# Kernel optimization log

Hardware: AMD Instinct MI355X
Metric: run time of the kernel (lower is better)

Reference implementation:

```python
import jax, jax.numpy as jnp
import numpy as np

B, T, D, H = 4, 1024, 1024, 16
DH = D // H
NEG_BIG = jnp.float32(-2.0**32 + 1)


def layer_norm(x, scale, bias, eps=1e-5):
    mean = jnp.mean(x, axis=-1, keepdims=True)
    var = jnp.mean(jnp.square(x - mean), axis=-1, keepdims=True)
    return (x - mean) * jax.lax.rsqrt(var + eps) * scale + bias


def setup_inputs() -> dict:
    key = jax.random.key(0)
    ks = jax.random.split(key, 10)
    s = 0.02
    x = jax.random.normal(ks[0], (B, T, D), jnp.float32)
    mask = jax.random.randint(ks[1], (B, T), 0, 2).astype(jnp.float32)
    return {
        "x": x,
        "mask": mask,
        "wq": jax.random.normal(ks[2], (D, D), jnp.float32) * s,
        "wk": jax.random.normal(ks[3], (D, D), jnp.float32) * s,
        "wv": jax.random.normal(ks[4], (D, D), jnp.float32) * s,
        "w1": jax.random.normal(ks[5], (D, D), jnp.float32) * s,
        "b1": jnp.zeros((D,), jnp.float32),
        "w2": jax.random.normal(ks[6], (D, D), jnp.float32) * s,
        "b2": jnp.zeros((D,), jnp.float32),
        "ln1_s": jnp.ones((D,), jnp.float32),
        "ln1_b": jnp.zeros((D,), jnp.float32),
        "ln2_s": jnp.ones((D,), jnp.float32),
        "ln2_b": jnp.zeros((D,), jnp.float32),
        "ln3_s": jnp.ones((D,), jnp.float32),
        "ln3_b": jnp.zeros((D,), jnp.float32),
    }


def _mask_enc(x, mask, wq, wk, wv, w1, b1, w2, b2,
              ln1_s, ln1_b, ln2_s, ln2_b, ln3_s, ln3_b):
    b, t, d = x.shape
    # --- multi-head attention (hand-rolled, matches torch split/cat trick) ---
    Q = (x @ wq).reshape(b, t, H, DH).transpose(0, 2, 1, 3)  # [B,H,T,dh]
    K = (x @ wk).reshape(b, t, H, DH).transpose(0, 2, 1, 3)
    V = (x @ wv).reshape(b, t, H, DH).transpose(0, 2, 1, 3)
    scores = jnp.einsum('bhqd,bhkd->bhqk', Q, K) / jnp.sqrt(jnp.float32(DH))
    # key padding mask from sign of |K| row sums
    key_m = jnp.sign(jnp.sum(jnp.abs(K), axis=-1))  # [B,H,T]
    scores = jnp.where(key_m[:, :, None, :] == 0, NEG_BIG, scores)
    # FORWARD direction: allowed where col_index > row_index (strict)
    idx = jnp.arange(t)
    allowed = (idx[None, :] > idx[:, None]).astype(scores.dtype)  # [T,T]
    scores = scores + (1.0 - allowed) * (-10000.0)
    attn = jax.nn.softmax(scores, axis=-1)
    # post-softmax query mask multiply
    query_m = jnp.sign(jnp.sum(jnp.abs(Q), axis=-1))[:, :, :, None]  # [B,H,T,1]
    attn = attn * query_m
    out = jnp.einsum('bhqk,bhkd->bhqd', attn, V)
    out = out.transpose(0, 2, 1, 3).reshape(b, t, d)  # combine heads
    out = out * mask[:, :, None]
    # --- residual + layernorm wrapper (attention) ---
    h1 = layer_norm(x + out, ln1_s, ln1_b)
    # --- FFN + residual + layernorm ---
    ffn = jax.nn.relu(h1 @ w1 + b1) @ w2 + b2
    h2 = layer_norm(h1 + ffn, ln2_s, ln2_b)
    # --- output normalization ---
    return layer_norm(h2, ln3_s, ln3_b)


def reference(x, mask, wq, wk, wv, w1, b1, w2, b2,
              ln1_s, ln1_b, ln2_s, ln2_b, ln3_s, ln3_b):
    return _mask_enc(x, mask, wq, wk, wv, w1, b1, w2, b2,
                     ln1_s, ln1_b, ln2_s, ln2_b, ln3_s, ln3_b)
```

## Files before the change

### kernel.cpp

```cpp
#include <hip/hip_runtime.h>
#include <stdint.h>


#define B_  4
#define T_  1024
#define D_  1024
#define H_  16
#define DH_ 64

typedef __attribute__((ext_vector_type(8))) short short8;
typedef __attribute__((ext_vector_type(4))) float floatx4;
typedef __attribute__((ext_vector_type(4))) _Float16 half4;

__device__ __forceinline__ unsigned short f2bf(float f) {
  union { float f; uint32_t u; } a; a.f = f;
  uint32_t r = a.u + 0x7FFFu + ((a.u >> 16) & 1u);
  return (unsigned short)(r >> 16);
}
__device__ __forceinline__ float bf2f(unsigned short u) {
  union { uint32_t u; float f; } a; a.u = ((uint32_t)u) << 16;
  return a.f;
}

#define GLD_LDS16(g, l) __builtin_amdgcn_global_load_lds( \
    (const __attribute__((address_space(1))) unsigned int*)(g), \
    (__attribute__((address_space(3))) unsigned int*)(l), 16, 0, 0)

__global__ __launch_bounds__(256)
void prep_kernel(const float4* __restrict__ x4, unsigned short* __restrict__ xb,
                 const float* __restrict__ w0, const float* __restrict__ w1,
                 const float* __restrict__ w2, const float* __restrict__ w3,
                 const float* __restrict__ w4, unsigned short* __restrict__ dst_all) {
  const int t = threadIdx.x;
  if (blockIdx.x < 4096) {
    int idx = blockIdx.x * 256 + t;
    float4 v = x4[idx];
    union { uint2 u; unsigned short s[4]; } o;
    o.s[0] = f2bf(v.x); o.s[1] = f2bf(v.y); o.s[2] = f2bf(v.z); o.s[3] = f2bf(v.w);
    *(uint2*)&xb[(size_t)idx * 4] = o.u;
    return;
  }
  const int b = blockIdx.x - 4096;
  const int z = b >> 8, ky = (b >> 4) & 15, nx = b & 15;
  const float* src = (z == 0) ? w0 : (z == 1) ? w1 : (z == 2) ? w2 : (z == 3) ? w3 : w4;
  unsigned short* dst = dst_all + (size_t)z * D_ * D_;
  __shared__ __align__(16) unsigned short tile[64 * 72];
  const int k0 = ky * 64, n0 = nx * 64;
#pragma unroll
  for (int c = 0; c < 4; ++c) {
    int idx = c * 256 + t;
    int r = idx >> 4, cc = (idx & 15) << 2;
    float4 v = *(const float4*)&src[(size_t)(k0 + r) * D_ + n0 + cc];
    tile[(cc + 0) * 72 + r] = f2bf(v.x);
    tile[(cc + 1) * 72 + r] = f2bf(v.y);
    tile[(cc + 2) * 72 + r] = f2bf(v.z);
    tile[(cc + 3) * 72 + r] = f2bf(v.w);
  }
  __syncthreads();
  int rr = t >> 2, ck = (t & 3) << 4;
  uint4 v0 = *(const uint4*)&tile[rr * 72 + ck];
  uint4 v1 = *(const uint4*)&tile[rr * 72 + ck + 8];
  *(uint4*)&dst[(size_t)(n0 + rr) * D_ + k0 + ck] = v0;
  *(uint4*)&dst[(size_t)(n0 + rr) * D_ + k0 + ck + 8] = v1;
}

__global__ __launch_bounds__(256, 2)
void gemm_qkv(const unsigned short* __restrict__ A,
              const unsigned short* __restrict__ Bt,
              unsigned short* __restrict__ oQ, unsigned short* __restrict__ oK,
              _Float16* __restrict__ oV) {
  const int K = 1024;
  __shared__ __align__(16) unsigned short As[128 * 32];
  __shared__ __align__(16) unsigned short Bs[128 * 32];
  __shared__ __align__(16) _Float16 Cs[2 * 64 * 136];
  const int t = threadIdx.x;
  const int lane = t & 63, w = t >> 6;
  const int quad = lane >> 4, lm = lane & 15;
  const int wm = w >> 1, wn = w & 1;
  const int m0 = blockIdx.y * 128, n0 = blockIdx.x * 128;
  const int arow = w * 32 + (lane >> 2), acol = (lane & 3) << 3;

  floatx4 acc[4][4];
#pragma unroll
  for (int i = 0; i < 4; ++i)
#pragma unroll
    for (int j = 0; j < 4; ++j) acc[i][j] = (floatx4){0.f, 0.f, 0.f, 0.f};

  for (int kt = 0; kt < K; kt += 32) {
    const unsigned short* ga = A + (size_t)(m0 + arow) * K + kt + acol;
    const unsigned short* gb = Bt + (size_t)(n0 + arow) * K + kt + acol;
    GLD_LDS16(ga, &As[(w * 32) * 32]);
    GLD_LDS16(ga + (size_t)16 * K, &As[(w * 32 + 16) * 32]);
    GLD_LDS16(gb, &Bs[(w * 32) * 32]);
    GLD_LDS16(gb + (size_t)16 * K, &Bs[(w * 32 + 16) * 32]);
    __syncthreads();
    short8 a[4], b[4];
#pragma unroll
    for (int i = 0; i < 4; ++i) a[i] = *(const short8*)&As[(wm * 64 + i * 16 + lm) * 32 + quad * 8];
#pragma unroll
    for (int j = 0; j < 4; ++j) b[j] = *(const short8*)&Bs[(wn * 64 + j * 16 + lm) * 32 + quad * 8];
#pragma unroll
    for (int i = 0; i < 4; ++i)
#pragma unroll
      for (int j = 0; j < 4; ++j)
        acc[i][j] = __builtin_amdgcn_mfma_f32_16x16x32_bf16(a[i], b[j], acc[i][j], 0, 0, 0);
    __syncthreads();
  }

  if (n0 < 2048) {
    unsigned short* p = (n0 < 1024) ? oQ : oK;
    const float qscale = (n0 < 1024) ? 0.18033688f : 1.0f;
#pragma unroll
    for (int i = 0; i < 4; ++i) {
      int gmb = m0 + wm * 64 + i * 16 + quad * 4;
#pragma unroll
      for (int j = 0; j < 4; ++j) {
        int gn = n0 + wn * 64 + j * 16 + lm;
        int nn = gn & 1023, hh = nn >> 6, dd = nn & 63;
#pragma unroll
        for (int r = 0; r < 4; ++r) {
          int gm = gmb + r;
          int bb = gm >> 10, tt = gm & 1023;
          p[(((size_t)bb * H_ + hh) * T_ + tt) * DH_ + dd] = f2bf(acc[i][j][r] * qscale);
        }
      }
    }
  } else {
#pragma unroll
    for (int i = 0; i < 4; ++i) {
#pragma unroll
      for (int j = 0; j < 4; ++j) {
        int gn = n0 + wn * 64 + j * 16 + lm;
        int hd = (gn >> 6) & 1, dd = gn & 63;
        int kperm = quad * 32 + (wm * 4 + i) * 4;
        union { _Float16 h[4]; uint2 u; } pk;
#pragma unroll
        for (int r = 0; r < 4; ++r) pk.h[r] = (_Float16)acc[i][j][r];
        *(uint2*)&Cs[((size_t)(hd * 64 + dd)) * 136 + kperm] = pk.u;
      }
    }
    __syncthreads();
    const int row = t >> 1, half = t & 1;
    const int hd = row >> 6, dd = row & 63;
    const int hh = ((n0 & 1023) >> 6) + hd;
    const int bb = m0 >> 10, kbg = (m0 >> 7) & 7;
    const _Float16* srcp = &Cs[(size_t)(hd * 64 + dd) * 136 + half * 64];
    _Float16* dstp = oV + ((((size_t)bb * H_ + hh) * DH_ + dd) * 8 + kbg) * 128 + half * 64;
#pragma unroll
    for (int g = 0; g < 8; ++g)
      *(uint4*)(dstp + g * 8) = *(const uint4*)(srcp + g * 8);
  }
}

template <int MODE>
__global__ __launch_bounds__(256, 2)
void gemm_ffn(const unsigned short* __restrict__ A,
              const unsigned short* __restrict__ Bt,
              unsigned short* __restrict__ oBf, float* __restrict__ oF,
              const float* __restrict__ bias) {
  const int K = 1024, N = 1024;
  __shared__ __align__(16) unsigned short As[64 * 32];
  __shared__ __align__(16) unsigned short Bs[128 * 32];
  const int t = threadIdx.x;
  const int lane = t & 63, w = t >> 6;
  const int quad = lane >> 4, lm = lane & 15;
  const int wm = w >> 1, wn = w & 1;
  const int m0 = blockIdx.y * 64, n0 = blockIdx.x * 128;
  const int lrow = lane >> 2, lcol = (lane & 3) << 3;

  floatx4 acc[2][4];
#pragma unroll
  for (int i = 0; i < 2; ++i)
#pragma unroll
    for (int j = 0; j < 4; ++j) acc[i][j] = (floatx4){0.f, 0.f, 0.f, 0.f};

  for (int kt = 0; kt < K; kt += 32) {
    const unsigned short* ga = A + (size_t)(m0 + w * 16 + lrow) * K + kt + lcol;
    const unsigned short* gb = Bt + (size_t)(n0 + w * 32 + lrow) * K + kt + lcol;
    GLD_LDS16(ga, &As[(w * 16) * 32]);
    GLD_LDS16(gb, &Bs[(w * 32) * 32]);
    GLD_LDS16(gb + (size_t)16 * K, &Bs[(w * 32 + 16) * 32]);
    __syncthreads();
    short8 a[2], b[4];
#pragma unroll
    for (int i = 0; i < 2; ++i) a[i] = *(const short8*)&As[(wm * 32 + i * 16 + lm) * 32 + quad * 8];
#pragma unroll
    for (int j = 0; j < 4; ++j) b[j] = *(const short8*)&Bs[(wn * 64 + j * 16 + lm) * 32 + quad * 8];
#pragma unroll
    for (int i = 0; i < 2; ++i)
#pragma unroll
      for (int j = 0; j < 4; ++j)
        acc[i][j] = __builtin_amdgcn_mfma_f32_16x16x32_bf16(a[i], b[j], acc[i][j], 0, 0, 0);
    __syncthreads();
  }

#pragma unroll
  for (int i = 0; i < 2; ++i) {
    int gmb = m0 + wm * 32 + i * 16 + quad * 4;
#pragma unroll
    for (int j = 0; j < 4; ++j) {
      int gn = n0 + wn * 64 + j * 16 + lm;
      float bv = bias[gn];
#pragma unroll
      for (int r = 0; r < 4; ++r) {
        int gm = gmb + r;
        float v = acc[i][j][r] + bv;
        if (MODE == 1) {
          oBf[(size_t)gm * N + gn] = f2bf(fmaxf(v, 0.f));
        } else {
          oF[(size_t)gm * N + gn] = v;
        }
      }
    }
  }
}

__global__ __launch_bounds__(256)
void flash_attn(const unsigned short* __restrict__ Qb,
                const unsigned short* __restrict__ Kb,
                const _Float16* __restrict__ Vtg,
                const float* __restrict__ maskp,
                unsigned short* __restrict__ attn) {
  const int t = threadIdx.x;
  const int lane = t & 63, w = t >> 6;
  const int quad = lane >> 4, lm = lane & 15;

  const int bid = blockIdx.x;
  const int hi = bid >> 8, lo = bid & 255;
  const int qraw = lo & 7;
  const int qb = hi ? (7 - qraw) : qraw;
  const int hb = (lo >> 3) | (hi << 5);
  const int hh = hb & 15, bb = hb >> 4;
  const int q0 = qb << 7;

  const size_t headoff = ((size_t)bb * H_ + hh) * T_ * DH_;
  const unsigned short* Qh = Qb + headoff;
  const unsigned short* Kh = Kb + headoff;
  const _Float16* Vh = Vtg + headoff;

  short8 qf[2][2];
#pragma unroll
  for (int qg = 0; qg < 2; ++qg)
#pragma unroll
    for (int ks = 0; ks < 2; ++ks)
      qf[qg][ks] = *(const short8*)(Qh + (size_t)(q0 + w * 32 + qg * 16 + lm) * 64 + ks * 32 + quad * 8);

  float lsum[2] = {0.f, 0.f};
  floatx4 acc[2][4];
#pragma unroll
  for (int qg = 0; qg < 2; ++qg)
#pragma unroll
    for (int j2 = 0; j2 < 4; ++j2) acc[qg][j2] = (floatx4){0.f, 0.f, 0.f, 0.f};

  const int qglob0 = q0 + w * 32 + lm;
  const bool excl1 = (qglob0 + 16 == 1023);
  const float MSHIFT = 14426.950408f;

  const int kb_lo = (qb == 7 && w == 3) ? 0 : qb;

  short8 kf[8][2];
  {
    const unsigned short* Kblk = Kh + (size_t)(kb_lo * 128) * 64;
#pragma unroll
    for (int j = 0; j < 8; ++j) {
      kf[j][0] = *(const short8*)(Kblk + (size_t)(j * 16 + lm) * 64 + quad * 8);
      kf[j][1] = *(const short8*)(Kblk + (size_t)(j * 16 + lm) * 64 + 32 + quad * 8);
    }
  }

  for (int kb = kb_lo; kb < 8; ++kb) {
    const int k0 = kb * 128;
    const bool need_mask = (kb <= qb);
    const bool has_next = (kb + 1 < 8);
    const unsigned short* Kn = Kh + (size_t)((kb + 1) * 128) * 64;

    union { uint4 u[4]; _Float16 h[32]; } vf[4];
#pragma unroll
    for (int j2 = 0; j2 < 4; ++j2) {
      const _Float16* vp = Vh + ((size_t)(j2 * 16 + lm) * 8 + kb) * 128 + quad * 32;
#pragma unroll
      for (int g = 0; g < 4; ++g) vf[j2].u[g] = *(const uint4*)(vp + g * 8);
    }

#pragma unroll
    for (int j = 0; j < 8; ++j) {
      floatx4 st[2];
#pragma unroll
      for (int qg = 0; qg < 2; ++qg) {
        floatx4 z = (floatx4){0.f, 0.f, 0.f, 0.f};
        z = __builtin_amdgcn_mfma_f32_16x16x32_bf16(kf[j][0], qf[qg][0], z, 0, 0, 0);
        st[qg] = __builtin_amdgcn_mfma_f32_16x16x32_bf16(kf[j][1], qf[qg][1], z, 0, 0, 0);
      }
      if (has_next) {
        kf[j][0] = *(const short8*)(Kn + (size_t)(j * 16 + lm) * 64 + quad * 8);
        kf[j][1] = *(const short8*)(Kn + (size_t)(j * 16 + lm) * 64 + 32 + quad * 8);
      }
      half4 pa[2];
#pragma unroll
      for (int qg = 0; qg < 2; ++qg) {
        const int qq = qglob0 + qg * 16;
        const bool skip = (qg == 1) && excl1;
#pragma unroll
        for (int r = 0; r < 4; ++r) {
          int kg = k0 + j * 16 + quad * 4 + r;
          float v = st[qg][r];
          if (need_mask && !skip && kg <= qq) v -= MSHIFT;
          float p = __builtin_amdgcn_exp2f(v);
          lsum[qg] += p;
          pa[qg][r] = (_Float16)p;
        }
      }
#pragma unroll
      for (int j2 = 0; j2 < 4; ++j2) {
        half4 vb;
#pragma unroll
        for (int r = 0; r < 4; ++r) vb[r] = vf[j2].h[j * 4 + r];
        acc[0][j2] = __builtin_amdgcn_mfma_f32_16x16x16f16(pa[0], vb, acc[0][j2], 0, 0, 0);
        acc[1][j2] = __builtin_amdgcn_mfma_f32_16x16x16f16(pa[1], vb, acc[1][j2], 0, 0, 0);
      }
    }
  }

#pragma unroll
  for (int qg = 0; qg < 2; ++qg) {
    float l = lsum[qg];
    l += __shfl_xor(l, 16);
    l += __shfl_xor(l, 32);
    float s = maskp[bb * T_ + qglob0 + qg * 16] / l;
#pragma unroll
    for (int r = 0; r < 4; ++r) {
      float bsc = __shfl(s, quad * 4 + r);
      int tq = q0 + w * 32 + qg * 16 + quad * 4 + r;
#pragma unroll
      for (int j2 = 0; j2 < 4; ++j2)
        attn[((size_t)(bb * T_ + tq)) * D_ + hh * 64 + j2 * 16 + lm] = f2bf(acc[qg][j2][r] * bsc);
    }
  }
}

__global__ __launch_bounds__(256)
void ln_res_kernel(const float* __restrict__ xa, const unsigned short* __restrict__ attn,
                   const float* __restrict__ sc, const float* __restrict__ bi,
                   float* __restrict__ h, unsigned short* __restrict__ hb) {
  const int row = blockIdx.x, t = threadIdx.x;
  const int lane = t & 63, wid = t >> 6;
  size_t base = (size_t)row * D_ + t * 4;
  float4 a = *(const float4*)&xa[base];
  union { uint2 u; unsigned short s[4]; } au;
  au.u = *(const uint2*)&attn[base];
  float v0 = a.x + bf2f(au.s[0]), v1 = a.y + bf2f(au.s[1]);
  float v2 = a.z + bf2f(au.s[2]), v3 = a.w + bf2f(au.s[3]);
  float s1 = v0 + v1 + v2 + v3;
  float s2 = v0 * v0 + v1 * v1 + v2 * v2 + v3 * v3;
#pragma unroll
  for (int off = 32; off; off >>= 1) { s1 += __shfl_down(s1, off); s2 += __shfl_down(s2, off); }
  __shared__ float r1[4], r2[4];
  if (lane == 0) { r1[wid] = s1; r2[wid] = s2; }
  __syncthreads();
  s1 = r1[0] + r1[1] + r1[2] + r1[3];
  s2 = r2[0] + r2[1] + r2[2] + r2[3];
  float mean = s1 * (1.f / 1024.f);
  float var = s2 * (1.f / 1024.f) - mean * mean;
  float rstd = rsqrtf(var + 1e-5f);
  float4 sv = *(const float4*)&sc[t * 4];
  float4 bv = *(const float4*)&bi[t * 4];
  float o0 = (v0 - mean) * rstd * sv.x + bv.x;
  float o1 = (v1 - mean) * rstd * sv.y + bv.y;
  float o2 = (v2 - mean) * rstd * sv.z + bv.z;
  float o3 = (v3 - mean) * rstd * sv.w + bv.w;
  float4 ov = {o0, o1, o2, o3};
  *(float4*)&h[base] = ov;
  union { uint2 u; unsigned short s[4]; } ob;
  ob.s[0] = f2bf(o0); ob.s[1] = f2bf(o1); ob.s[2] = f2bf(o2); ob.s[3] = f2bf(o3);
  *(uint2*)&hb[base] = ob.u;
}

__global__ __launch_bounds__(256)
void ln_double_kernel(const float* __restrict__ h1, const float* __restrict__ ffn,
                      const float* __restrict__ s2c, const float* __restrict__ b2c,
                      const float* __restrict__ s3c, const float* __restrict__ b3c,
                      float* __restrict__ out) {
  const int row = blockIdx.x, t = threadIdx.x;
  const int lane = t & 63, wid = t >> 6;
  size_t base = (size_t)row * D_ + t * 4;
  float4 a = *(const float4*)&h1[base];
  float4 b = *(const float4*)&ffn[base];
  float v0 = a.x + b.x, v1 = a.y + b.y, v2 = a.z + b.z, v3 = a.w + b.w;
  float s1 = v0 + v1 + v2 + v3;
  float s2 = v0 * v0 + v1 * v1 + v2 * v2 + v3 * v3;
#pragma unroll
  for (int off = 32; off; off >>= 1) { s1 += __shfl_down(s1, off); s2 += __shfl_down(s2, off); }
  __shared__ float ra[4], rb[4], rc[4], rd[4];
  if (lane == 0) { ra[wid] = s1; rb[wid] = s2; }
  __syncthreads();
  s1 = ra[0] + ra[1] + ra[2] + ra[3];
  s2 = rb[0] + rb[1] + rb[2] + rb[3];
  float mean = s1 * (1.f / 1024.f);
  float var = s2 * (1.f / 1024.f) - mean * mean;
  float rstd = rsqrtf(var + 1e-5f);
  float4 sv = *(const float4*)&s2c[t * 4];
  float4 bv = *(const float4*)&b2c[t * 4];
  float o0 = (v0 - mean) * rstd * sv.x + bv.x;
  float o1 = (v1 - mean) * rstd * sv.y + bv.y;
  float o2 = (v2 - mean) * rstd * sv.z + bv.z;
  float o3 = (v3 - mean) * rstd * sv.w + bv.w;
  float u1 = o0 + o1 + o2 + o3;
  float u2 = o0 * o0 + o1 * o1 + o2 * o2 + o3 * o3;
#pragma unroll
  for (int off = 32; off; off >>= 1) { u1 += __shfl_down(u1, off); u2 += __shfl_down(u2, off); }
  if (lane == 0) { rc[wid] = u1; rd[wid] = u2; }
  __syncthreads();
  u1 = rc[0] + rc[1] + rc[2] + rc[3];
  u2 = rd[0] + rd[1] + rd[2] + rd[3];
  float mean2 = u1 * (1.f / 1024.f);
  float var2 = u2 * (1.f / 1024.f) - mean2 * mean2;
  float rstd2 = rsqrtf(var2 + 1e-5f);
  float4 s3v = *(const float4*)&s3c[t * 4];
  float4 b3v = *(const float4*)&b3c[t * 4];
  float4 fo;
  fo.x = (o0 - mean2) * rstd2 * s3v.x + b3v.x;
  fo.y = (o1 - mean2) * rstd2 * s3v.y + b3v.y;
  fo.z = (o2 - mean2) * rstd2 * s3v.z + b3v.z;
  fo.w = (o3 - mean2) * rstd2 * s3v.w + b3v.w;
  *(float4*)&out[base] = fo;
}

extern "C" void kernel_launch(void* const* d_in, const int* in_sizes, int n_in,
                              void* d_out, int out_size, void* d_ws, size_t ws_size,
                              hipStream_t stream) {
  (void)in_sizes; (void)n_in; (void)out_size; (void)ws_size;
  const float* x   = (const float*)d_in[0];
  const float* msk = (const float*)d_in[1];
  const float* wq  = (const float*)d_in[2];
  const float* wk  = (const float*)d_in[3];
  const float* wv  = (const float*)d_in[4];
  const float* w1  = (const float*)d_in[5];
  const float* b1  = (const float*)d_in[6];
  const float* w2  = (const float*)d_in[7];
  const float* b2  = (const float*)d_in[8];
  const float* l1s = (const float*)d_in[9];
  const float* l1b = (const float*)d_in[10];
  const float* l2s = (const float*)d_in[11];
  const float* l2b = (const float*)d_in[12];
  const float* l3s = (const float*)d_in[13];
  const float* l3b = (const float*)d_in[14];
  float* outp = (float*)d_out;

  char* ws = (char*)d_ws;
  unsigned short* xb   = (unsigned short*)(ws);
  unsigned short* wt   = (unsigned short*)(ws + ((size_t)8  << 20));
  unsigned short* Qb   = (unsigned short*)(ws + ((size_t)18 << 20));
  unsigned short* Kb   = (unsigned short*)(ws + ((size_t)26 << 20));
  _Float16*       Vtg  = (_Float16*)(ws + ((size_t)34 << 20));
  unsigned short* attn = (unsigned short*)(ws + ((size_t)42 << 20));
  float* h1            = (float*)(ws + ((size_t)50 << 20));
  unsigned short* h1b  = (unsigned short*)(ws + ((size_t)18 << 20));
  unsigned short* gb   = (unsigned short*)(ws + ((size_t)26 << 20));
  float* ffn           = (float*)(ws + ((size_t)34 << 20));

  prep_kernel<<<4096 + 1280, 256, 0, stream>>>((const float4*)x, xb,
                                               wq, wk, wv, w1, w2, wt);
  gemm_qkv<<<dim3(24, 32), 256, 0, stream>>>(xb, wt, Qb, Kb, Vtg);
  flash_attn<<<512, 256, 0, stream>>>(Qb, Kb, Vtg, msk, attn);
  ln_res_kernel<<<4096, 256, 0, stream>>>(x, attn, l1s, l1b, h1, h1b);
  gemm_ffn<1><<<dim3(8, 64), 256, 0, stream>>>(h1b, wt + (size_t)3 * 1024 * 1024, gb, nullptr, b1);
  gemm_ffn<2><<<dim3(8, 64), 256, 0, stream>>>(gb, wt + (size_t)4 * 1024 * 1024, nullptr, ffn, b2);
  ln_double_kernel<<<4096, 256, 0, stream>>>(h1, ffn, l2s, l2b, l3s, l3b, outp);
}
```

Before: 248.7 us.

## Split flash-attention key range across two wave groups and combine via LDS

Doubles the flash_attn block to 512 threads, with the second group of four waves handling the upper half of the key blocks for the same query rows. Partial accumulators and row sums are merged through shared memory before normalization and store. Block-to-head mapping is also reordered so that blocks landing on the same XCD share a head, aiming for better L2 reuse of K/V. This roughly halves per-wave serial work to cut the critical path, at the cost of an LDS reduction, a barrier, and higher register pressure under launch_bounds(512,4).

```diff
diff --git a/kernel.cpp b/kernel.cpp
--- a/kernel.cpp
+++ b/kernel.cpp
@@ -215,7 +215,7 @@
   }
 }
 
-__global__ __launch_bounds__(256)
+__global__ __launch_bounds__(512, 4)
 void flash_attn(const unsigned short* __restrict__ Qb,
                 const unsigned short* __restrict__ Kb,
                 const _Float16* __restrict__ Vtg,
@@ -224,13 +224,16 @@
   const int t = threadIdx.x;
   const int lane = t & 63, w = t >> 6;
   const int quad = lane >> 4, lm = lane & 15;
+  const int qw = w & 3, kh = w >> 2;
 
   const int bid = blockIdx.x;
-  const int hi = bid >> 8, lo = bid & 255;
-  const int qraw = lo & 7;
-  const int qb = hi ? (7 - qraw) : qraw;
-  const int hb = (lo >> 3) | (hi << 5);
-  const int hh = hb & 15, bb = hb >> 4;
+  const int xcd = bid & 7;
+  const int qslot = (bid >> 3) & 7;
+  const int hgrp = bid >> 6;
+  const int head = hgrp * 8 + xcd;
+  const int qh = qslot >> 1;
+  const int qb = (qslot & 1) ? 7 - qh : qh;
+  const int hh = head & 15, bb = head >> 4;
   const int q0 = qb << 7;
 
   const size_t headoff = ((size_t)bb * H_ + hh) * T_ * DH_;
@@ -243,7 +246,7 @@
   for (int qg = 0; qg < 2; ++qg)
 #pragma unroll
     for (int ks = 0; ks < 2; ++ks)
-      qf[qg][ks] = *(const short8*)(Qh + (size_t)(q0 + w * 32 + qg * 16 + lm) * 64 + ks * 32 + quad * 8);
+      qf[qg][ks] = *(const short8*)(Qh + (size_t)(q0 + qw * 32 + qg * 16 + lm) * 64 + ks * 32 + quad * 8);
 
   float lsum[2] = {0.f, 0.f};
   floatx4 acc[2][4];
@@ -252,15 +255,19 @@
 #pragma unroll
     for (int j2 = 0; j2 < 4; ++j2) acc[qg][j2] = (floatx4){0.f, 0.f, 0.f, 0.f};
 
-  const int qglob0 = q0 + w * 32 + lm;
+  const int qglob0 = q0 + qw * 32 + lm;
   const bool excl1 = (qglob0 + 16 == 1023);
   const float MSHIFT = 14426.950408f;
 
-  const int kb_lo = (qb == 7 && w == 3) ? 0 : qb;
+  const int kb_lo = (qb == 7 && qw == 3) ? 0 : qb;
+  const int cnt = 8 - kb_lo;
+  const int halfc = (cnt + 1) >> 1;
+  const int kb_begin = kh ? kb_lo + halfc : kb_lo;
+  const int kb_end   = kh ? 8 : kb_lo + halfc;
 
   short8 kf[8][2];
-  {
-    const unsigned short* Kblk = Kh + (size_t)(kb_lo * 128) * 64;
+  if (kb_begin < kb_end) {
+    const unsigned short* Kblk = Kh + (size_t)(kb_begin * 128) * 64;
 #pragma unroll
     for (int j = 0; j < 8; ++j) {
       kf[j][0] = *(const short8*)(Kblk + (size_t)(j * 16 + lm) * 64 + quad * 8);
@@ -268,10 +275,10 @@
     }
   }
 
-  for (int kb = kb_lo; kb < 8; ++kb) {
+  for (int kb = kb_begin; kb < kb_end; ++kb) {
     const int k0 = kb * 128;
     const bool need_mask = (kb <= qb);
-    const bool has_next = (kb + 1 < 8);
+    const bool has_next = (kb + 1 < kb_end);
     const unsigned short* Kn = Kh + (size_t)((kb + 1) * 128) * 64;
 
     union { uint4 u[4]; _Float16 h[32]; } vf[4];
@@ -321,6 +328,35 @@
     }
   }
 
+  __shared__ float comb[4][34][64];
+  if (kh == 1) {
+    float* p = &comb[qw][0][lane];
+#pragma unroll
+    for (int qg = 0; qg < 2; ++qg)
+#pragma unroll
+      for (int j2 = 0; j2 < 4; ++j2)
+#pragma unroll
+        for (int r = 0; r < 4; ++r)
+          p[((qg * 4 + j2) * 4 + r) * 64] = acc[qg][j2][r];
+    p[32 * 64] = lsum[0];
+    p[33 * 64] = lsum[1];
+  }
+  __syncthreads();
+  if (kh == 1) return;
+
+  {
+    const float* p = &comb[qw][0][lane];
+#pragma unroll
+    for (int qg = 0; qg < 2; ++qg)
+#pragma unroll
+      for (int j2 = 0; j2 < 4; ++j2)
+#pragma unroll
+        for (int r = 0; r < 4; ++r)
+          acc[qg][j2][r] += p[((qg * 4 + j2) * 4 + r) * 64];
+    lsum[0] += p[32 * 64];
+    lsum[1] += p[33 * 64];
+  }
+
 #pragma unroll
   for (int qg = 0; qg < 2; ++qg) {
     float l = lsum[qg];
@@ -330,7 +366,7 @@
 #pragma unroll
     for (int r = 0; r < 4; ++r) {
       float bsc = __shfl(s, quad * 4 + r);
-      int tq = q0 + w * 32 + qg * 16 + quad * 4 + r;
+      int tq = q0 + qw * 32 + qg * 16 + quad * 4 + r;
 #pragma unroll
       for (int j2 = 0; j2 < 4; ++j2)
         attn[((size_t)(bb * T_ + tq)) * D_ + hh * 64 + j2 * 16 + lm] = f2bf(acc[qg][j2][r] * bsc);
@@ -461,7 +497,7 @@
   prep_kernel<<<4096 + 1280, 256, 0, stream>>>((const float4*)x, xb,
                                                wq, wk, wv, w1, w2, wt);
   gemm_qkv<<<dim3(24, 32), 256, 0, stream>>>(xb, wt, Qb, Kb, Vtg);
-  flash_attn<<<512, 256, 0, stream>>>(Qb, Kb, Vtg, msk, attn);
+  flash_attn<<<512, 512, 0, stream>>>(Qb, Kb, Vtg, msk, attn);
   ln_res_kernel<<<4096, 256, 0, stream>>>(x, attn, l1s, l1b, h1, h1b);
   gemm_ffn<1><<<dim3(8, 64), 256, 0, stream>>>(h1b, wt + (size_t)3 * 1024 * 1024, gb, nullptr, b1);
   gemm_ffn<2><<<dim3(8, 64), 256, 0, stream>>>(gb, wt + (size_t)4 * 1024 * 1024, nullptr, ffn, b2);
```

Result: slower. 381.2 us (+53.2%).

## Split attention over key halves and merge partials in residual layernorm

Applied to the files above, without the earlier changes.

Doubles the flash-attention grid by splitting each query block's key range into two halves, writing unnormalized bf16 partial outputs and row sums to separate buffers. The residual layernorm kernel then sums the partials, divides by the combined row sum and applies the mask. Block indices are remapped so heads align with XCDs. This targets low occupancy and load imbalance of the causal attention at the cost of extra partial-buffer traffic and a second bf16 rounding.

```diff
diff --git a/kernel.cpp b/kernel.cpp
--- a/kernel.cpp
+++ b/kernel.cpp
@@ -219,18 +219,21 @@
 void flash_attn(const unsigned short* __restrict__ Qb,
                 const unsigned short* __restrict__ Kb,
                 const _Float16* __restrict__ Vtg,
-                const float* __restrict__ maskp,
-                unsigned short* __restrict__ attn) {
+                unsigned short* __restrict__ aP0, unsigned short* __restrict__ aP1,
+                float* __restrict__ lP0, float* __restrict__ lP1) {
   const int t = threadIdx.x;
   const int lane = t & 63, w = t >> 6;
   const int quad = lane >> 4, lm = lane & 15;
 
   const int bid = blockIdx.x;
-  const int hi = bid >> 8, lo = bid & 255;
-  const int qraw = lo & 7;
-  const int qb = hi ? (7 - qraw) : qraw;
-  const int hb = (lo >> 3) | (hi << 5);
-  const int hh = hb & 15, bb = hb >> 4;
+  const int xcd = bid & 7;
+  const int kh = (bid >> 3) & 1;
+  const int qslot = (bid >> 4) & 7;
+  const int hgrp = bid >> 7;
+  const int head = hgrp * 8 + xcd;
+  const int qh = qslot >> 1;
+  const int qb = (qslot & 1) ? 7 - qh : qh;
+  const int hh = head & 15, bb = head >> 4;
   const int q0 = qb << 7;
 
   const size_t headoff = ((size_t)bb * H_ + hh) * T_ * DH_;
@@ -257,10 +260,14 @@
   const float MSHIFT = 14426.950408f;
 
   const int kb_lo = (qb == 7 && w == 3) ? 0 : qb;
+  const int cnt = 8 - kb_lo;
+  const int halfc = (cnt + 1) >> 1;
+  const int kb_begin = kh ? kb_lo + halfc : kb_lo;
+  const int kb_end   = kh ? 8 : kb_lo + halfc;
 
   short8 kf[8][2];
-  {
-    const unsigned short* Kblk = Kh + (size_t)(kb_lo * 128) * 64;
+  if (kb_begin < kb_end) {
+    const unsigned short* Kblk = Kh + (size_t)(kb_begin * 128) * 64;
 #pragma unroll
     for (int j = 0; j < 8; ++j) {
       kf[j][0] = *(const short8*)(Kblk + (size_t)(j * 16 + lm) * 64 + quad * 8);
@@ -268,10 +275,10 @@
     }
   }
 
-  for (int kb = kb_lo; kb < 8; ++kb) {
+  for (int kb = kb_begin; kb < kb_end; ++kb) {
     const int k0 = kb * 128;
     const bool need_mask = (kb <= qb);
-    const bool has_next = (kb + 1 < 8);
+    const bool has_next = (kb + 1 < kb_end);
     const unsigned short* Kn = Kh + (size_t)((kb + 1) * 128) * 64;
 
     union { uint4 u[4]; _Float16 h[32]; } vf[4];
@@ -321,35 +328,49 @@
     }
   }
 
+  unsigned short* ap = kh ? aP1 : aP0;
+  float* lp = kh ? lP1 : lP0;
 #pragma unroll
   for (int qg = 0; qg < 2; ++qg) {
     float l = lsum[qg];
     l += __shfl_xor(l, 16);
     l += __shfl_xor(l, 32);
-    float s = maskp[bb * T_ + qglob0 + qg * 16] / l;
+    if (quad == 0)
+      lp[((size_t)bb * H_ + hh) * T_ + qglob0 + qg * 16] = l;
 #pragma unroll
     for (int r = 0; r < 4; ++r) {
-      float bsc = __shfl(s, quad * 4 + r);
       int tq = q0 + w * 32 + qg * 16 + quad * 4 + r;
 #pragma unroll
       for (int j2 = 0; j2 < 4; ++j2)
-        attn[((size_t)(bb * T_ + tq)) * D_ + hh * 64 + j2 * 16 + lm] = f2bf(acc[qg][j2][r] * bsc);
+        ap[((size_t)(bb * T_ + tq)) * D_ + hh * 64 + j2 * 16 + lm] = f2bf(acc[qg][j2][r]);
     }
   }
 }
 
 __global__ __launch_bounds__(256)
-void ln_res_kernel(const float* __restrict__ xa, const unsigned short* __restrict__ attn,
+void ln_res_kernel(const float* __restrict__ xa,
+                   const unsigned short* __restrict__ a0,
+                   const unsigned short* __restrict__ a1,
+                   const float* __restrict__ l0, const float* __restrict__ l1,
+                   const float* __restrict__ mk,
                    const float* __restrict__ sc, const float* __restrict__ bi,
                    float* __restrict__ h, unsigned short* __restrict__ hb) {
   const int row = blockIdx.x, t = threadIdx.x;
   const int lane = t & 63, wid = t >> 6;
+  const int bb = row >> 10, tt = row & 1023;
+  const int hh = t >> 4;
   size_t base = (size_t)row * D_ + t * 4;
   float4 a = *(const float4*)&xa[base];
-  union { uint2 u; unsigned short s[4]; } au;
-  au.u = *(const uint2*)&attn[base];
-  float v0 = a.x + bf2f(au.s[0]), v1 = a.y + bf2f(au.s[1]);
-  float v2 = a.z + bf2f(au.s[2]), v3 = a.w + bf2f(au.s[3]);
+  union { uint2 u; unsigned short s[4]; } u0, u1;
+  u0.u = *(const uint2*)&a0[base];
+  u1.u = *(const uint2*)&a1[base];
+  size_t lidx = ((size_t)bb * H_ + hh) * T_ + tt;
+  float l = l0[lidx] + l1[lidx];
+  float s = mk[bb * T_ + tt] / l;
+  float v0 = a.x + (bf2f(u0.s[0]) + bf2f(u1.s[0])) * s;
+  float v1 = a.y + (bf2f(u0.s[1]) + bf2f(u1.s[1])) * s;
+  float v2 = a.z + (bf2f(u0.s[2]) + bf2f(u1.s[2])) * s;
+  float v3 = a.w + (bf2f(u0.s[3]) + bf2f(u1.s[3])) * s;
   float s1 = v0 + v1 + v2 + v3;
   float s2 = v0 * v0 + v1 * v1 + v2 * v2 + v3 * v3;
 #pragma unroll
@@ -452,17 +473,21 @@
   unsigned short* Qb   = (unsigned short*)(ws + ((size_t)18 << 20));
   unsigned short* Kb   = (unsigned short*)(ws + ((size_t)26 << 20));
   _Float16*       Vtg  = (_Float16*)(ws + ((size_t)34 << 20));
-  unsigned short* attn = (unsigned short*)(ws + ((size_t)42 << 20));
-  float* h1            = (float*)(ws + ((size_t)50 << 20));
+  unsigned short* aP0  = (unsigned short*)(ws + ((size_t)42 << 20));
+  unsigned short* aP1  = (unsigned short*)(ws + ((size_t)50 << 20));
+  float* lP0           = (float*)(ws);
+  float* lP1           = (float*)(ws + ((size_t)1 << 20));
   unsigned short* h1b  = (unsigned short*)(ws + ((size_t)18 << 20));
-  unsigned short* gb   = (unsigned short*)(ws + ((size_t)26 << 20));
-  float* ffn           = (float*)(ws + ((size_t)34 << 20));
+  float* h1            = (float*)(ws + ((size_t)26 << 20));
+  unsigned short* gb   = (unsigned short*)(ws + ((size_t)42 << 20));
+  float* ffn           = (float*)(ws + ((size_t)50 << 20));
 
   prep_kernel<<<4096 + 1280, 256, 0, stream>>>((const float4*)x, xb,
                                                wq, wk, wv, w1, w2, wt);
   gemm_qkv<<<dim3(24, 32), 256, 0, stream>>>(xb, wt, Qb, Kb, Vtg);
-  flash_attn<<<512, 256, 0, stream>>>(Qb, Kb, Vtg, msk, attn);
-  ln_res_kernel<<<4096, 256, 0, stream>>>(x, attn, l1s, l1b, h1, h1b);
+  flash_attn<<<1024, 256, 0, stream>>>(Qb, Kb, Vtg, aP0, aP1, lP0, lP1);
+  ln_res_kernel<<<4096, 256, 0, stream>>>(x, aP0, aP1, lP0, lP1, msk,
+                                          l1s, l1b, h1, h1b);
   gemm_ffn<1><<<dim3(8, 64), 256, 0, stream>>>(h1b, wt + (size_t)3 * 1024 * 1024, gb, nullptr, b1);
   gemm_ffn<2><<<dim3(8, 64), 256, 0, stream>>>(gb, wt + (size_t)4 * 1024 * 1024, nullptr, ffn, b2);
   ln_double_kernel<<<4096, 256, 0, stream>>>(h1, ffn, l2s, l2b, l3s, l3b, outp);
```

Result: slower. 267.1 us (+7.4%).
